# Kernel optimization log

Hardware: AMD Instinct MI355X
Metric: run time of the kernel (lower is better)

## Reference

```python
import jax, jax.numpy as jnp
import numpy as np

C = 512
NUM_HEADS = 8
HEAD_DIM = C // NUM_HEADS  # 64
BN_EPS = 1e-5


def setup_inputs() -> dict:
    key = jax.random.key(0)
    ks = jax.random.split(key, 12)
    B, H, W = 8, 32, 32
    s = 0.02
    return {
        "x": jax.random.normal(ks[0], (B, C, H, W), dtype=jnp.float32),
        "gamma": jnp.ones((C,), jnp.float32),
        "beta": jnp.zeros((C,), jnp.float32),
        "rmean": jnp.zeros((C,), jnp.float32),
        "rvar": jnp.ones((C,), jnp.float32),
        "wq": jax.random.normal(ks[1], (C, C), jnp.float32) * s,
        "bq": jnp.zeros((C,), jnp.float32),
        "wk": jax.random.normal(ks[2], (C, C), jnp.float32) * s,
        "bk": jnp.zeros((C,), jnp.float32),
        "wv": jax.random.normal(ks[3], (C, C), jnp.float32) * s,
        "bv": jnp.zeros((C,), jnp.float32),
        "wp": jax.random.normal(ks[4], (C, C), jnp.float32) * s,
        "bp": jnp.zeros((C,), jnp.float32),
    }


def _conv1x1(w, b, h):
    # 1x1 conv == per-pixel dense: (O,C) x (B,C,H,W) -> (B,O,H,W)
    return jnp.einsum('oc,bchw->bohw', w, h) + b[None, :, None, None]


def reference(x, gamma, beta, rmean, rvar, wq, bq, wk, bk, wv, bv, wp, bp):
    B, Cc, H, W = x.shape
    N = H * W
    # BatchNorm2d (eval mode, running stats)
    inv = gamma / jnp.sqrt(rvar + BN_EPS)
    h = x * inv[None, :, None, None] + (beta - rmean * inv)[None, :, None, None]
    q = _conv1x1(wq, bq, h).reshape(B, NUM_HEADS, HEAD_DIM, N)
    k = _conv1x1(wk, bk, h).reshape(B, NUM_HEADS, HEAD_DIM, N)
    v = _conv1x1(wv, bv, h).reshape(B, NUM_HEADS, HEAD_DIM, N)
    scale = 1.0 / np.sqrt(HEAD_DIM).astype(np.float32)
    attn = jnp.einsum('bhdn,bhdm->bhnm', q, k) * scale  # [B,heads,N,N]
    attn = jnp.clip(attn, -50.0, 50.0)
    attn = jax.nn.softmax(attn, axis=-1)
    out = jnp.einsum('bhnm,bhdm->bhdn', attn, v).reshape(B, Cc, H, W)
    out = _conv1x1(wp, bp, out)
    return x + out
```

## Files before the change

### kernel.cpp

```cpp
#include <hip/hip_runtime.h>
#include <stdint.h>

#define C_DIM 512
#define NHEADS 8
#define HDIM 64
#define BATCH 8
#define NPIX 1024
#define ATTN_SCALE 0.125f

typedef __bf16 bf16x8 __attribute__((ext_vector_type(8)));
typedef float f32x4 __attribute__((ext_vector_type(4)));

__device__ __forceinline__ unsigned short f2bf(float f) {
  union { float f; unsigned u; } v; v.f = f;
  unsigned r = v.u + 0x7fffu + ((v.u >> 16) & 1u);
  return (unsigned short)(r >> 16);
}

__device__ __forceinline__ void gl_lds16(const void* g, void* l) {
  __builtin_amdgcn_global_load_lds(
      (__attribute__((address_space(1))) void*)g,
      (__attribute__((address_space(3))) void*)l,
      16, 0, 0);
}

__global__ __launch_bounds__(256) void k_prep(const float* __restrict__ wq,
                                              const float* __restrict__ wk,
                                              const float* __restrict__ wv,
                                              const float* __restrict__ wp,
                                              unsigned short* __restrict__ wbf) {
  const int n = C_DIM * C_DIM;
  for (int i = blockIdx.x * blockDim.x + threadIdx.x; i < 4 * n;
       i += gridDim.x * blockDim.x) {
    const float* src = (i < n) ? wq : (i < 2 * n) ? wk : (i < 3 * n) ? wv : wp;
    wbf[i] = f2bf(src[i & (n - 1)]);
  }
}

__global__ __launch_bounds__(256) void k_bnT(const float* __restrict__ x,
                                             const float* __restrict__ gamma,
                                             const float* __restrict__ beta,
                                             const float* __restrict__ rmean,
                                             const float* __restrict__ rvar,
                                             unsigned short* __restrict__ hbT) {
  __shared__ unsigned short tile[64][72];
  const int b = blockIdx.z, c0 = blockIdx.y * 64, n0 = blockIdx.x * 64;
  const int t = threadIdx.x;
#pragma unroll
  for (int it = 0; it < 4; ++it) {
    int c = it * 16 + (t >> 4);
    int n = (t & 15) * 4;
    const float4 v = *(const float4*)&x[((size_t)b * C_DIM + c0 + c) * NPIX + n0 + n];
    int cc = c0 + c;
    float inv = gamma[cc] * rsqrtf(rvar[cc] + 1e-5f);
    float add = beta[cc] - rmean[cc] * inv;
    tile[c][n + 0] = f2bf(v.x * inv + add);
    tile[c][n + 1] = f2bf(v.y * inv + add);
    tile[c][n + 2] = f2bf(v.z * inv + add);
    tile[c][n + 3] = f2bf(v.w * inv + add);
  }
  __syncthreads();
#pragma unroll
  for (int it = 0; it < 2; ++it) {
    int n = it * 32 + (t >> 3);
    int cj = (t & 7) * 8;
    unsigned short tmp[8];
#pragma unroll
    for (int u = 0; u < 8; ++u) tmp[u] = tile[cj + u][n];
    uint4 pk;
    pk.x = (unsigned)tmp[0] | ((unsigned)tmp[1] << 16);
    pk.y = (unsigned)tmp[2] | ((unsigned)tmp[3] << 16);
    pk.z = (unsigned)tmp[4] | ((unsigned)tmp[5] << 16);
    pk.w = (unsigned)tmp[6] | ((unsigned)tmp[7] << 16);
    *(uint4*)&hbT[((size_t)b * NPIX + n0 + n) * C_DIM + c0 + cj] = pk;
  }
}

__global__ __launch_bounds__(256) void k_qkv(const unsigned short* __restrict__ wbf,
                                             const float* __restrict__ bq,
                                             const float* __restrict__ bk,
                                             const float* __restrict__ bv,
                                             const unsigned short* __restrict__ hbT,
                                             unsigned short* __restrict__ QT,
                                             unsigned short* __restrict__ KT,
                                             unsigned short* __restrict__ Vb) {
  __shared__ unsigned short Atile[128 * 32];
  __shared__ unsigned short Btile[128 * 32];
  const int which = blockIdx.z >> 3;
  const int b = blockIdx.z & 7;
  const int m0 = blockIdx.y * 128, n0 = blockIdx.x * 128;
  const unsigned short* W = wbf + (size_t)which * C_DIM * C_DIM;
  const int t = threadIdx.x, wave = t >> 6, lane = t & 63;
  const int wr = wave >> 1, wc = wave & 1;
  f32x4 acc[4][4] = {};

  const int st_row = lane >> 2;
  const int st_col = (((lane & 3) ^ ((lane >> 3) & 3))) * 8;

  for (int k0 = 0; k0 < C_DIM; k0 += 32) {
    __syncthreads();
#pragma unroll
    for (int it = 0; it < 2; ++it) {
      int q = wave + 4 * it;
      int row = q * 16 + st_row;
      gl_lds16(&W[(size_t)(m0 + row) * C_DIM + k0 + st_col], &Atile[q * 512]);
      gl_lds16(&hbT[((size_t)b * NPIX + n0 + row) * C_DIM + k0 + st_col], &Btile[q * 512]);
    }
    __syncthreads();
    bf16x8 af[4], bfr[4];
#pragma unroll
    for (int i = 0; i < 4; ++i) {
      int row = wr * 64 + i * 16 + (lane & 15);
      af[i] = *(const bf16x8*)&Atile[row * 32 + (((lane >> 4) ^ ((row >> 1) & 3)) * 8)];
    }
#pragma unroll
    for (int j = 0; j < 4; ++j) {
      int row = wc * 64 + j * 16 + (lane & 15);
      bfr[j] = *(const bf16x8*)&Btile[row * 32 + (((lane >> 4) ^ ((row >> 1) & 3)) * 8)];
    }
#pragma unroll
    for (int i = 0; i < 4; ++i)
#pragma unroll
      for (int j = 0; j < 4; ++j)
        acc[i][j] = __builtin_amdgcn_mfma_f32_16x16x32_bf16(af[i], bfr[j], acc[i][j], 0, 0, 0);
  }

  const float* bias = (which == 0) ? bq : (which == 1) ? bk : bv;
  if (which < 2) {
    unsigned short* T = (which == 0) ? QT : KT;
#pragma unroll
    for (int i = 0; i < 4; ++i) {
      int o = m0 + wr * 64 + i * 16 + (lane >> 4) * 4;
      float b0 = bias[o + 0], b1 = bias[o + 1], b2 = bias[o + 2], b3 = bias[o + 3];
#pragma unroll
      for (int j = 0; j < 4; ++j) {
        int n = n0 + wc * 64 + j * 16 + (lane & 15);
        ushort4 pk;
        pk.x = f2bf(acc[i][j][0] + b0);
        pk.y = f2bf(acc[i][j][1] + b1);
        pk.z = f2bf(acc[i][j][2] + b2);
        pk.w = f2bf(acc[i][j][3] + b3);
        *(ushort4*)&T[((size_t)b * NPIX + n) * C_DIM + o] = pk;
      }
    }
  } else {
#pragma unroll
    for (int i = 0; i < 4; ++i) {
      int o = m0 + wr * 64 + i * 16 + (lane >> 4) * 4;
#pragma unroll
      for (int j = 0; j < 4; ++j) {
        int n = n0 + wc * 64 + j * 16 + (lane & 15);
#pragma unroll
        for (int r = 0; r < 4; ++r)
          Vb[((size_t)b * C_DIM + o + r) * NPIX + n] = f2bf(acc[i][j][r] + bias[o + r]);
      }
    }
  }
}

__global__ __launch_bounds__(256) void k_attn(const unsigned short* __restrict__ QT,
                                              const unsigned short* __restrict__ KT,
                                              const unsigned short* __restrict__ Vb,
                                              unsigned short* __restrict__ AOT) {
  __shared__ unsigned short Qs[128 * 64];
  __shared__ unsigned short Ks[128 * 64];
  __shared__ unsigned short Vs[64 * 128];
  __shared__ unsigned short Ps[4][32 * 136];
  __shared__ float rs_lds[128];

  const int b = blockIdx.z, h = blockIdx.y, n0 = blockIdx.x * 128;
  const int t = threadIdx.x, wave = t >> 6, lane = t & 63;

  const int qk_row = lane >> 3;
  const int qk_col = ((lane & 7) ^ (lane >> 3)) * 8;

#pragma unroll
  for (int it = 0; it < 4; ++it) {
    int q = wave + 4 * it;
    gl_lds16(&QT[((size_t)b * NPIX + n0 + q * 8 + qk_row) * C_DIM + h * HDIM + qk_col],
             &Qs[q * 512]);
  }

  f32x4 oacc[2][4] = {};
  float rsum[2][4] = {};

  for (int m0 = 0; m0 < NPIX; m0 += 128) {
    __syncthreads();
#pragma unroll
    for (int it = 0; it < 4; ++it) {
      int q = wave + 4 * it;
      gl_lds16(&KT[((size_t)b * NPIX + m0 + q * 8 + qk_row) * C_DIM + h * HDIM + qk_col],
               &Ks[q * 512]);
    }
#pragma unroll
    for (int it = 0; it < 4; ++it) {
      int q = wave + 4 * it;
      int row = q * 4 + (lane >> 4);
      int col = ((lane & 15) ^ (((q & 1) * 4) + (lane >> 4))) * 8;
      gl_lds16(&Vb[((size_t)b * C_DIM + h * HDIM + row) * NPIX + m0 + col], &Vs[q * 512]);
    }
    __syncthreads();

    f32x4 s[2][8] = {};
#pragma unroll
    for (int kk = 0; kk < 2; ++kk) {
      bf16x8 aq[2], bk8[8];
#pragma unroll
      for (int i = 0; i < 2; ++i) {
        int row = wave * 32 + i * 16 + (lane & 15);
        aq[i] = *(const bf16x8*)&Qs[row * 64 + (((kk * 4 + (lane >> 4)) ^ (row & 7)) * 8)];
      }
#pragma unroll
      for (int j = 0; j < 8; ++j) {
        int row = j * 16 + (lane & 15);
        bk8[j] = *(const bf16x8*)&Ks[row * 64 + (((kk * 4 + (lane >> 4)) ^ (row & 7)) * 8)];
      }
#pragma unroll
      for (int i = 0; i < 2; ++i)
#pragma unroll
        for (int j = 0; j < 8; ++j)
          s[i][j] = __builtin_amdgcn_mfma_f32_16x16x32_bf16(aq[i], bk8[j], s[i][j], 0, 0, 0);
    }

#pragma unroll
    for (int i = 0; i < 2; ++i)
#pragma unroll
      for (int j = 0; j < 8; ++j)
#pragma unroll
        for (int r = 0; r < 4; ++r) {
          float e = __expf(fminf(fmaxf(s[i][j][r] * ATTN_SCALE, -50.f), 50.f));
          rsum[i][r] += e;
          Ps[wave][(i * 16 + (lane >> 4) * 4 + r) * 136 + j * 16 + (lane & 15)] = f2bf(e);
        }
    __syncthreads();

#pragma unroll
    for (int kk = 0; kk < 4; ++kk) {
      bf16x8 av[4], bp8[2];
#pragma unroll
      for (int dj = 0; dj < 4; ++dj) {
        int row = dj * 16 + (lane & 15);
        av[dj] = *(const bf16x8*)&Vs[row * 128 + (((kk * 4 + (lane >> 4)) ^ (row & 7)) * 8)];
      }
#pragma unroll
      for (int ai = 0; ai < 2; ++ai)
        bp8[ai] = *(const bf16x8*)&Ps[wave][(ai * 16 + (lane & 15)) * 136 + kk * 32 + (lane >> 4) * 8];
#pragma unroll
      for (int ai = 0; ai < 2; ++ai)
#pragma unroll
        for (int dj = 0; dj < 4; ++dj)
          oacc[ai][dj] = __builtin_amdgcn_mfma_f32_16x16x32_bf16(av[dj], bp8[ai], oacc[ai][dj], 0, 0, 0);
    }
  }

#pragma unroll
  for (int i = 0; i < 2; ++i)
#pragma unroll
    for (int r = 0; r < 4; ++r) {
      float v = rsum[i][r];
      v += __shfl_xor(v, 1);
      v += __shfl_xor(v, 2);
      v += __shfl_xor(v, 4);
      v += __shfl_xor(v, 8);
      rsum[i][r] = v;
    }
  if ((lane & 15) == 0) {
#pragma unroll
    for (int i = 0; i < 2; ++i)
#pragma unroll
      for (int r = 0; r < 4; ++r)
        rs_lds[wave * 32 + i * 16 + (lane >> 4) * 4 + r] = rsum[i][r];
  }
  __syncthreads();

#pragma unroll
  for (int ai = 0; ai < 2; ++ai) {
    float inv = 1.0f / rs_lds[wave * 32 + ai * 16 + (lane & 15)];
    int n = n0 + wave * 32 + ai * 16 + (lane & 15);
#pragma unroll
    for (int dj = 0; dj < 4; ++dj) {
      ushort4 pk;
      pk.x = f2bf(oacc[ai][dj][0] * inv);
      pk.y = f2bf(oacc[ai][dj][1] * inv);
      pk.z = f2bf(oacc[ai][dj][2] * inv);
      pk.w = f2bf(oacc[ai][dj][3] * inv);
      *(ushort4*)&AOT[((size_t)b * NPIX + n) * C_DIM + h * HDIM + dj * 16 + (lane >> 4) * 4] = pk;
    }
  }
}

__global__ __launch_bounds__(256) void k_proj(const unsigned short* __restrict__ Wp,
                                              const float* __restrict__ bp,
                                              const unsigned short* __restrict__ AOT,
                                              const float* __restrict__ x,
                                              float* __restrict__ out) {
  __shared__ unsigned short Atile[128 * 32];
  __shared__ unsigned short Btile[128 * 32];
  const int b = blockIdx.z;
  const int m0 = blockIdx.y * 128, n0 = blockIdx.x * 128;
  const int t = threadIdx.x, wave = t >> 6, lane = t & 63;
  const int wr = wave >> 1, wc = wave & 1;
  f32x4 acc[4][4] = {};
  const int st_row = lane >> 2;
  const int st_col = (((lane & 3) ^ ((lane >> 3) & 3))) * 8;

  for (int k0 = 0; k0 < C_DIM; k0 += 32) {
    __syncthreads();
#pragma unroll
    for (int it = 0; it < 2; ++it) {
      int q = wave + 4 * it;
      int row = q * 16 + st_row;
      gl_lds16(&Wp[(size_t)(m0 + row) * C_DIM + k0 + st_col], &Atile[q * 512]);
      gl_lds16(&AOT[((size_t)b * NPIX + n0 + row) * C_DIM + k0 + st_col], &Btile[q * 512]);
    }
    __syncthreads();
    bf16x8 af[4], bfr[4];
#pragma unroll
    for (int i = 0; i < 4; ++i) {
      int row = wr * 64 + i * 16 + (lane & 15);
      af[i] = *(const bf16x8*)&Atile[row * 32 + (((lane >> 4) ^ ((row >> 1) & 3)) * 8)];
    }
#pragma unroll
    for (int j = 0; j < 4; ++j) {
      int row = wc * 64 + j * 16 + (lane & 15);
      bfr[j] = *(const bf16x8*)&Btile[row * 32 + (((lane >> 4) ^ ((row >> 1) & 3)) * 8)];
    }
#pragma unroll
    for (int i = 0; i < 4; ++i)
#pragma unroll
      for (int j = 0; j < 4; ++j)
        acc[i][j] = __builtin_amdgcn_mfma_f32_16x16x32_bf16(af[i], bfr[j], acc[i][j], 0, 0, 0);
  }

#pragma unroll
  for (int i = 0; i < 4; ++i) {
    int o = m0 + wr * 64 + i * 16 + (lane >> 4) * 4;
    float b0 = bp[o + 0], b1 = bp[o + 1], b2 = bp[o + 2], b3 = bp[o + 3];
#pragma unroll
    for (int j = 0; j < 4; ++j) {
      int n = n0 + wc * 64 + j * 16 + (lane & 15);
      size_t base = ((size_t)b * C_DIM + o) * NPIX + n;
      out[base + 0 * NPIX] = acc[i][j][0] + b0 + x[base + 0 * NPIX];
      out[base + 1 * NPIX] = acc[i][j][1] + b1 + x[base + 1 * NPIX];
      out[base + 2 * NPIX] = acc[i][j][2] + b2 + x[base + 2 * NPIX];
      out[base + 3 * NPIX] = acc[i][j][3] + b3 + x[base + 3 * NPIX];
    }
  }
}

extern "C" void kernel_launch(void* const* d_in, const int* in_sizes, int n_in,
                              void* d_out, int out_size, void* d_ws, size_t ws_size,
                              hipStream_t stream) {
  (void)in_sizes; (void)n_in; (void)out_size; (void)ws_size;
  const float* x     = (const float*)d_in[0];
  const float* gamma = (const float*)d_in[1];
  const float* beta  = (const float*)d_in[2];
  const float* rmean = (const float*)d_in[3];
  const float* rvar  = (const float*)d_in[4];
  const float* wq    = (const float*)d_in[5];
  const float* bq    = (const float*)d_in[6];
  const float* wk    = (const float*)d_in[7];
  const float* bk    = (const float*)d_in[8];
  const float* wv    = (const float*)d_in[9];
  const float* bv    = (const float*)d_in[10];
  const float* wp    = (const float*)d_in[11];
  const float* bp    = (const float*)d_in[12];

  unsigned short* ws  = (unsigned short*)d_ws;
  const size_t WSZ    = (size_t)C_DIM * C_DIM;
  const size_t BIG    = (size_t)BATCH * NPIX * C_DIM;
  unsigned short* wbf = ws;
  unsigned short* hbT = wbf + 4 * WSZ;
  unsigned short* QT  = hbT + BIG;
  unsigned short* KT  = QT + BIG;
  unsigned short* Vb  = KT + BIG;
  unsigned short* AOT = Vb + BIG;

  k_prep<<<dim3(512), dim3(256), 0, stream>>>(wq, wk, wv, wp, wbf);
  k_bnT<<<dim3(16, 8, 8), dim3(256), 0, stream>>>(x, gamma, beta, rmean, rvar, hbT);
  k_qkv<<<dim3(8, 4, 24), dim3(256), 0, stream>>>(wbf, bq, bk, bv, hbT, QT, KT, Vb);
  k_attn<<<dim3(8, 8, 8), dim3(256), 0, stream>>>(QT, KT, Vb, AOT);
  k_proj<<<dim3(8, 4, 8), dim3(256), 0, stream>>>(wbf + 3 * WSZ, bp, AOT, x, (float*)d_out);
}
```

Before: 195.2 us.

## Rewrite attention with 32x32 MFMA, register-resident P, and double-buffered K/V

The attention kernel is restructured. Q is now scaled by scale*log2e in the QKV epilogue so softmax can use exp2f with a rescaled clip bound. Attention switches to 32x32x16 MFMAs computing S^T, so the P tile stays in registers via cvt_pk and permlane32_swap instead of a round trip through LDS. K and V tiles are double-buffered so the next tile loads while the current one computes, and the grid is flattened with batch in the low bits. This removes the P LDS traffic and two barriers per tile, at the cost of more LDS for the double buffers and extra bf16 rounding of the prescaled Q.

```diff
diff --git a/kernel.cpp b/kernel.cpp
--- a/kernel.cpp
+++ b/kernel.cpp
@@ -6,10 +6,12 @@
 #define HDIM 64
 #define BATCH 8
 #define NPIX 1024
-#define ATTN_SCALE 0.125f
+#define Q_PRESCALE 0.18033688011112042f
+#define CLIP_LOG2 72.13475204444817f
 
 typedef __bf16 bf16x8 __attribute__((ext_vector_type(8)));
 typedef float f32x4 __attribute__((ext_vector_type(4)));
+typedef float f32x16 __attribute__((ext_vector_type(16)));
 
 __device__ __forceinline__ unsigned short f2bf(float f) {
   union { float f; unsigned u; } v; v.f = f;
@@ -128,6 +130,7 @@
   const float* bias = (which == 0) ? bq : (which == 1) ? bk : bv;
   if (which < 2) {
     unsigned short* T = (which == 0) ? QT : KT;
+    const float qs = (which == 0) ? Q_PRESCALE : 1.0f;
 #pragma unroll
     for (int i = 0; i < 4; ++i) {
       int o = m0 + wr * 64 + i * 16 + (lane >> 4) * 4;
@@ -136,10 +139,10 @@
       for (int j = 0; j < 4; ++j) {
         int n = n0 + wc * 64 + j * 16 + (lane & 15);
         ushort4 pk;
-        pk.x = f2bf(acc[i][j][0] + b0);
-        pk.y = f2bf(acc[i][j][1] + b1);
-        pk.z = f2bf(acc[i][j][2] + b2);
-        pk.w = f2bf(acc[i][j][3] + b3);
+        pk.x = f2bf((acc[i][j][0] + b0) * qs);
+        pk.y = f2bf((acc[i][j][1] + b1) * qs);
+        pk.z = f2bf((acc[i][j][2] + b2) * qs);
+        pk.w = f2bf((acc[i][j][3] + b3) * qs);
         *(ushort4*)&T[((size_t)b * NPIX + n) * C_DIM + o] = pk;
       }
     }
@@ -162,131 +165,111 @@
                                               const unsigned short* __restrict__ KT,
                                               const unsigned short* __restrict__ Vb,
                                               unsigned short* __restrict__ AOT) {
-  __shared__ unsigned short Qs[128 * 64];
-  __shared__ unsigned short Ks[128 * 64];
-  __shared__ unsigned short Vs[64 * 128];
-  __shared__ unsigned short Ps[4][32 * 136];
+  __shared__ unsigned short Ks[2][128 * 64];
+  __shared__ unsigned short Vs[2][64 * 128];
   __shared__ float rs_lds[128];
 
-  const int b = blockIdx.z, h = blockIdx.y, n0 = blockIdx.x * 128;
-  const int t = threadIdx.x, wave = t >> 6, lane = t & 63;
-
-  const int qk_row = lane >> 3;
-  const int qk_col = ((lane & 7) ^ (lane >> 3)) * 8;
-
-#pragma unroll
-  for (int it = 0; it < 4; ++it) {
-    int q = wave + 4 * it;
-    gl_lds16(&QT[((size_t)b * NPIX + n0 + q * 8 + qk_row) * C_DIM + h * HDIM + qk_col],
-             &Qs[q * 512]);
-  }
-
-  f32x4 oacc[2][4] = {};
-  float rsum[2][4] = {};
-
-  for (int m0 = 0; m0 < NPIX; m0 += 128) {
-    __syncthreads();
+  const int bid = blockIdx.x;
+  const int b = bid & 7, h = (bid >> 3) & 7, qt = bid >> 6;
+  const int n0 = qt * 128;
+  const int lane = threadIdx.x & 63, wave = threadIdx.x >> 6;
+  const int l31 = lane & 31, hi = lane >> 5;
+
+  bf16x8 qf[4];
+  {
+    const unsigned short* qbase =
+        QT + ((size_t)b * NPIX + n0 + wave * 32 + l31) * C_DIM + h * HDIM + hi * 8;
+#pragma unroll
+    for (int kk = 0; kk < 4; ++kk) qf[kk] = *(const bf16x8*)(qbase + kk * 16);
+  }
+
+  auto stage = [&](int buf, int tile) {
+    const int m0 = tile * 128;
 #pragma unroll
     for (int it = 0; it < 4; ++it) {
-      int q = wave + 4 * it;
-      gl_lds16(&KT[((size_t)b * NPIX + m0 + q * 8 + qk_row) * C_DIM + h * HDIM + qk_col],
-               &Ks[q * 512]);
+      int rb = it * 32 + wave * 8;
+      int row = rb + (lane >> 3);
+      int srcc = ((lane & 7) ^ (row & 7)) * 8;
+      gl_lds16(&KT[((size_t)b * NPIX + m0 + row) * C_DIM + h * HDIM + srcc],
+               &Ks[buf][rb * 64]);
     }
 #pragma unroll
     for (int it = 0; it < 4; ++it) {
-      int q = wave + 4 * it;
-      int row = q * 4 + (lane >> 4);
-      int col = ((lane & 15) ^ (((q & 1) * 4) + (lane >> 4))) * 8;
-      gl_lds16(&Vb[((size_t)b * C_DIM + h * HDIM + row) * NPIX + m0 + col], &Vs[q * 512]);
-    }
-    __syncthreads();
-
-    f32x4 s[2][8] = {};
-#pragma unroll
-    for (int kk = 0; kk < 2; ++kk) {
-      bf16x8 aq[2], bk8[8];
-#pragma unroll
-      for (int i = 0; i < 2; ++i) {
-        int row = wave * 32 + i * 16 + (lane & 15);
-        aq[i] = *(const bf16x8*)&Qs[row * 64 + (((kk * 4 + (lane >> 4)) ^ (row & 7)) * 8)];
-      }
-#pragma unroll
-      for (int j = 0; j < 8; ++j) {
-        int row = j * 16 + (lane & 15);
-        bk8[j] = *(const bf16x8*)&Ks[row * 64 + (((kk * 4 + (lane >> 4)) ^ (row & 7)) * 8)];
-      }
-#pragma unroll
-      for (int i = 0; i < 2; ++i)
-#pragma unroll
-        for (int j = 0; j < 8; ++j)
-          s[i][j] = __builtin_amdgcn_mfma_f32_16x16x32_bf16(aq[i], bk8[j], s[i][j], 0, 0, 0);
-    }
-
-#pragma unroll
-    for (int i = 0; i < 2; ++i)
-#pragma unroll
-      for (int j = 0; j < 8; ++j)
-#pragma unroll
-        for (int r = 0; r < 4; ++r) {
-          float e = __expf(fminf(fmaxf(s[i][j][r] * ATTN_SCALE, -50.f), 50.f));
-          rsum[i][r] += e;
-          Ps[wave][(i * 16 + (lane >> 4) * 4 + r) * 136 + j * 16 + (lane & 15)] = f2bf(e);
-        }
-    __syncthreads();
-
-#pragma unroll
-    for (int kk = 0; kk < 4; ++kk) {
-      bf16x8 av[4], bp8[2];
-#pragma unroll
-      for (int dj = 0; dj < 4; ++dj) {
-        int row = dj * 16 + (lane & 15);
-        av[dj] = *(const bf16x8*)&Vs[row * 128 + (((kk * 4 + (lane >> 4)) ^ (row & 7)) * 8)];
-      }
-#pragma unroll
-      for (int ai = 0; ai < 2; ++ai)
-        bp8[ai] = *(const bf16x8*)&Ps[wave][(ai * 16 + (lane & 15)) * 136 + kk * 32 + (lane >> 4) * 8];
-#pragma unroll
-      for (int ai = 0; ai < 2; ++ai)
-#pragma unroll
-        for (int dj = 0; dj < 4; ++dj)
-          oacc[ai][dj] = __builtin_amdgcn_mfma_f32_16x16x32_bf16(av[dj], bp8[ai], oacc[ai][dj], 0, 0, 0);
-    }
-  }
-
-#pragma unroll
-  for (int i = 0; i < 2; ++i)
-#pragma unroll
-    for (int r = 0; r < 4; ++r) {
-      float v = rsum[i][r];
-      v += __shfl_xor(v, 1);
-      v += __shfl_xor(v, 2);
-      v += __shfl_xor(v, 4);
-      v += __shfl_xor(v, 8);
-      rsum[i][r] = v;
-    }
-  if ((lane & 15) == 0) {
-#pragma unroll
-    for (int i = 0; i < 2; ++i)
-#pragma unroll
-      for (int r = 0; r < 4; ++r)
-        rs_lds[wave * 32 + i * 16 + (lane >> 4) * 4 + r] = rsum[i][r];
-  }
+      int rb = it * 16 + wave * 4;
+      int d = rb + (lane >> 4);
+      int srck = ((lane & 15) ^ (d & 7)) * 8;
+      gl_lds16(&Vb[((size_t)b * C_DIM + h * HDIM + d) * NPIX + m0 + srck],
+               &Vs[buf][rb * 128]);
+    }
+  };
+
+  f32x16 oacc[2] = {};
+  float rs0 = 0.f, rs1 = 0.f;
+
+  stage(0, 0);
   __syncthreads();
 
-#pragma unroll
-  for (int ai = 0; ai < 2; ++ai) {
-    float inv = 1.0f / rs_lds[wave * 32 + ai * 16 + (lane & 15)];
-    int n = n0 + wave * 32 + ai * 16 + (lane & 15);
-#pragma unroll
-    for (int dj = 0; dj < 4; ++dj) {
-      ushort4 pk;
-      pk.x = f2bf(oacc[ai][dj][0] * inv);
-      pk.y = f2bf(oacc[ai][dj][1] * inv);
-      pk.z = f2bf(oacc[ai][dj][2] * inv);
-      pk.w = f2bf(oacc[ai][dj][3] * inv);
-      *(ushort4*)&AOT[((size_t)b * NPIX + n) * C_DIM + h * HDIM + dj * 16 + (lane >> 4) * 4] = pk;
-    }
-  }
+  for (int tile = 0; tile < 8; ++tile) {
+    const int cur = tile & 1;
+    if (tile < 7) stage(cur ^ 1, tile + 1);
+
+#pragma unroll
+    for (int kt = 0; kt < 4; ++kt) {
+      f32x16 s = {};
+#pragma unroll
+      for (int kk = 0; kk < 4; ++kk) {
+        int row = kt * 32 + l31;
+        int phys = (kk * 2 + hi) ^ (row & 7);
+        bf16x8 kf = *(const bf16x8*)&Ks[cur][row * 64 + phys * 8];
+        s = __builtin_amdgcn_mfma_f32_32x32x16_bf16(kf, qf[kk], s, 0, 0, 0);
+      }
+      unsigned w[8];
+#pragma unroll
+      for (int r2 = 0; r2 < 8; ++r2) {
+        float e0 = exp2f(fminf(fmaxf(s[2 * r2], -CLIP_LOG2), CLIP_LOG2));
+        float e1 = exp2f(fminf(fmaxf(s[2 * r2 + 1], -CLIP_LOG2), CLIP_LOG2));
+        rs0 += e0;
+        rs1 += e1;
+        asm("v_cvt_pk_bf16_f32 %0, %1, %2" : "=v"(w[r2]) : "v"(e0), "v"(e1));
+      }
+      asm volatile("v_permlane32_swap_b32 %0, %1" : "+v"(w[0]), "+v"(w[2]));
+      asm volatile("v_permlane32_swap_b32 %0, %1" : "+v"(w[1]), "+v"(w[3]));
+      asm volatile("v_permlane32_swap_b32 %0, %1" : "+v"(w[4]), "+v"(w[6]));
+      asm volatile("v_permlane32_swap_b32 %0, %1" : "+v"(w[5]), "+v"(w[7]));
+      union U8 { unsigned u[4]; bf16x8 v; };
+      U8 pa0, pa1;
+      pa0.u[0] = w[0]; pa0.u[1] = w[1]; pa0.u[2] = w[2]; pa0.u[3] = w[3];
+      pa1.u[0] = w[4]; pa1.u[1] = w[5]; pa1.u[2] = w[6]; pa1.u[3] = w[7];
+#pragma unroll
+      for (int dt = 0; dt < 2; ++dt) {
+        int d = dt * 32 + l31;
+        bf16x8 v0 = *(const bf16x8*)&Vs[cur][d * 128 + (((kt * 4 + hi) ^ (d & 7)) * 8)];
+        bf16x8 v1 = *(const bf16x8*)&Vs[cur][d * 128 + (((kt * 4 + 2 + hi) ^ (d & 7)) * 8)];
+        oacc[dt] = __builtin_amdgcn_mfma_f32_32x32x16_bf16(pa0.v, v0, oacc[dt], 0, 0, 0);
+        oacc[dt] = __builtin_amdgcn_mfma_f32_32x32x16_bf16(pa1.v, v1, oacc[dt], 0, 0, 0);
+      }
+    }
+    __syncthreads();
+  }
+
+  float tot = rs0 + rs1;
+  tot += __shfl_xor(tot, 32);
+  if (lane < 32) rs_lds[wave * 32 + lane] = tot;
+
+  float inv[16];
+#pragma unroll
+  for (int r = 0; r < 16; ++r)
+    inv[r] = 1.0f / rs_lds[wave * 32 + (r & 3) + 8 * (r >> 2) + 4 * hi];
+
+  __bf16* obase = (__bf16*)(AOT + ((size_t)b * NPIX + n0 + wave * 32) * C_DIM +
+                            h * HDIM + l31);
+#pragma unroll
+  for (int dt = 0; dt < 2; ++dt)
+#pragma unroll
+    for (int r = 0; r < 16; ++r) {
+      int q = (r & 3) + 8 * (r >> 2) + 4 * hi;
+      obase[(size_t)q * C_DIM + dt * 32] = (__bf16)(oacc[dt][r] * inv[r]);
+    }
 }
 
 __global__ __launch_bounds__(256) void k_proj(const unsigned short* __restrict__ Wp,
@@ -379,6 +362,6 @@
   k_prep<<<dim3(512), dim3(256), 0, stream>>>(wq, wk, wv, wp, wbf);
   k_bnT<<<dim3(16, 8, 8), dim3(256), 0, stream>>>(x, gamma, beta, rmean, rvar, hbT);
   k_qkv<<<dim3(8, 4, 24), dim3(256), 0, stream>>>(wbf, bq, bk, bv, hbT, QT, KT, Vb);
-  k_attn<<<dim3(8, 8, 8), dim3(256), 0, stream>>>(QT, KT, Vb, AOT);
+  k_attn<<<dim3(512), dim3(256), 0, stream>>>(QT, KT, Vb, AOT);
   k_proj<<<dim3(8, 4, 8), dim3(256), 0, stream>>>(wbf + 3 * WSZ, bp, AOT, x, (float*)d_out);
 }
```

Measured after the change: 173.4 us. 1.13x faster.
